# Kernel optimization log

Hardware: AMD Instinct MI355X
Metric: run time of the kernel (lower is better)

## Reference

```python
import jax, jax.numpy as jnp
import numpy as np

B, S, D, H = 2, 2048, 1024, 16
DEPTH = D // H
NEG = -1e9


def setup_inputs() -> dict:
    key = jax.random.key(0)
    ks = jax.random.split(key, 8)
    scale = 1.0 / np.sqrt(D)
    inp = {
        "query": jax.random.normal(ks[0], (B, S, D), jnp.float32),
        "key": jax.random.normal(ks[1], (B, S, D), jnp.float32),
        "value": jax.random.normal(ks[2], (B, S, D), jnp.float32),
        # causal look-ahead mask: 1 where attention is disallowed
        "mask": (1.0 - jnp.tril(jnp.ones((S, S), jnp.float32)))[None, None, :, :],
        "Wq": jax.random.normal(ks[3], (D, D), jnp.float32) * scale,
        "Wk": jax.random.normal(ks[4], (D, D), jnp.float32) * scale,
        "Wv": jax.random.normal(ks[5], (D, D), jnp.float32) * scale,
        "Wo": jax.random.normal(ks[6], (D, D), jnp.float32) * scale,
        "bq": jnp.zeros((D,), jnp.float32),
        "bk": jnp.zeros((D,), jnp.float32),
        "bv": jnp.zeros((D,), jnp.float32),
        "bo": jnp.zeros((D,), jnp.float32),
    }
    return inp


def _split_heads(x):
    # [B,S,D] -> [B,H,S,depth]
    return x.reshape(B, -1, H, DEPTH).transpose(0, 2, 1, 3)


def reference(query, key, value, mask, Wq, Wk, Wv, Wo, bq, bk, bv, bo):
    q = _split_heads(query @ Wq + bq)
    k = _split_heads(key @ Wk + bk)
    v = _split_heads(value @ Wv + bv)
    logits = jnp.einsum("bhqd,bhkd->bhqk", q, k) / jnp.sqrt(jnp.float32(DEPTH))
    logits = logits + mask * NEG
    attn = jax.nn.softmax(logits, axis=-1)
    ctx = jnp.einsum("bhqk,bhkd->bhqd", attn, v)  # [B,H,S,depth]
    concat = ctx.transpose(0, 2, 1, 3).reshape(B, -1, D)
    return concat @ Wo + bo
```

## Files before the change

### kernel.cpp

```cpp
#include <hip/hip_runtime.h>
#include <hip/hip_bf16.h>
#include <stdint.h>

#define BB 2
#define SS 2048
#define DDIM 1024
#define HH 16
#define DEPTH 64
#define MROWS (BB*SS)

typedef short bf16x8 __attribute__((ext_vector_type(8)));
typedef float f32x4 __attribute__((ext_vector_type(4)));

__device__ inline ushort f2bf(float f) {
  union { float f; unsigned u; } v; v.f = f;
  unsigned r = v.u + 0x7fffu + ((v.u >> 16) & 1u);
  return (ushort)(r >> 16);
}

__device__ inline uint pkbf(float a, float b) {
  uint r;
  asm("v_cvt_pk_bf16_f32 %0, %1, %2" : "=v"(r) : "v"(a), "v"(b));
  return r;
}

__device__ inline void gload_lds16(const void* g, void* l) {
  __builtin_amdgcn_global_load_lds(
      (const __attribute__((address_space(1))) unsigned*)g,
      (__attribute__((address_space(3))) unsigned*)l,
      16, 0, 0);
}

__global__ void wprep_kernel(const float* __restrict__ W0, const float* __restrict__ W1,
                             const float* __restrict__ W2, const float* __restrict__ W3,
                             ushort* __restrict__ T0, ushort* __restrict__ T1,
                             ushort* __restrict__ T2, ushort* __restrict__ T3) {
  __shared__ float tile[32][33];
  int z = blockIdx.x >> 10;
  int rr = blockIdx.x & 1023;
  const float* W = (z == 0) ? W0 : (z == 1) ? W1 : (z == 2) ? W2 : W3;
  ushort* T = (z == 0) ? T0 : (z == 1) ? T1 : (z == 2) ? T2 : T3;
  int tx = threadIdx.x & 31, ty = threadIdx.x >> 5;
  int n0 = (rr & 31) * 32, k0 = (rr >> 5) * 32;
#pragma unroll
  for (int i = 0; i < 4; i++)
    tile[ty + i * 8][tx] = W[(size_t)(k0 + ty + i * 8) * DDIM + n0 + tx];
  __syncthreads();
#pragma unroll
  for (int i = 0; i < 4; i++)
    T[(size_t)(n0 + ty + i * 8) * DDIM + k0 + tx] = f2bf(tile[tx][ty + i * 8]);
}

__global__ __launch_bounds__(256, 3) void qkv_gemm_kernel(
    const float* __restrict__ Aq, const float* __restrict__ Ak, const float* __restrict__ Av,
    const ushort* __restrict__ Wqt, const ushort* __restrict__ Wkt, const ushort* __restrict__ Wvt,
    const float* __restrict__ bqp, const float* __restrict__ bkp, const float* __restrict__ bvp,
    ushort* __restrict__ Qh, ushort* __restrict__ Kh, ushort* __restrict__ Vtg) {
  const int id = blockIdx.x;
  const int xcd = id & 7;
  const int rest = id >> 3;
  const int xblk = rest & 7;
  const int slot = rest >> 3;
  const int g = xcd * 12 + slot;
  const int yblk = g & 31;
  const int z = g >> 5;

  const float*  Ap = (z == 0) ? Aq  : (z == 1) ? Ak  : Av;
  const ushort* Bt = (z == 0) ? Wqt : (z == 1) ? Wkt : Wvt;
  const float* bias = (z == 0) ? bqp : (z == 1) ? bkp : bvp;

  __shared__ __align__(16) ushort As[128 * 64];
  __shared__ __align__(16) ushort Bs[2][128 * 64];
  const int tid = threadIdx.x;
  const int w = tid >> 6, lane = tid & 63;
  const int m0 = yblk * 128, n0 = xblk * 128;
  const int wr = (w >> 1) * 64, wc = (w & 1) * 64;
  const int l4 = lane >> 4, l15 = lane & 15;
  const int row16 = tid >> 4;
  const int col4 = (tid & 15) * 4;
  const int srow8 = w * 8 + (lane >> 3);
  const int scol8 = (lane & 7) * 8;

  f32x4 zero = {0.f, 0.f, 0.f, 0.f};
  f32x4 acc[4][4];
#pragma unroll
  for (int i = 0; i < 4; i++)
#pragma unroll
    for (int j = 0; j < 4; j++) acc[i][j] = zero;

  float4 areg[8];
#pragma unroll
  for (int j = 0; j < 8; ++j)
    areg[j] = *(const float4*)&Ap[(size_t)(m0 + j * 16 + row16) * DDIM + col4];
#pragma unroll
  for (int it = 0; it < 4; ++it)
    gload_lds16(Bt + (size_t)(n0 + it * 32 + srow8) * DDIM + scol8,
                &Bs[0][(it * 32 + w * 8) * 64]);
#pragma unroll
  for (int j = 0; j < 8; ++j) {
    uint2 pk;
    pk.x = pkbf(areg[j].x, areg[j].y);
    pk.y = pkbf(areg[j].z, areg[j].w);
    *(uint2*)&As[(j * 16 + row16) * 64 + col4] = pk;
  }
  __syncthreads();

  int buf = 0;
  for (int t = 0; t < 16; ++t) {
    if (t + 1 < 16) {
#pragma unroll
      for (int it = 0; it < 4; ++it)
        gload_lds16(Bt + (size_t)(n0 + it * 32 + srow8) * DDIM + (t + 1) * 64 + scol8,
                    &Bs[buf ^ 1][(it * 32 + w * 8) * 64]);
#pragma unroll
      for (int j = 0; j < 8; ++j)
        areg[j] = *(const float4*)&Ap[(size_t)(m0 + j * 16 + row16) * DDIM + (t + 1) * 64 + col4];
    }
#pragma unroll
    for (int kk = 0; kk < 2; ++kk) {
      bf16x8 af[4], bfr[4];
#pragma unroll
      for (int m = 0; m < 4; m++)
        af[m] = *(const bf16x8*)&As[(wr + m * 16 + l15) * 64 + kk * 32 + l4 * 8];
#pragma unroll
      for (int n = 0; n < 4; n++)
        bfr[n] = *(const bf16x8*)&Bs[buf][(wc + n * 16 + l15) * 64 + kk * 32 + l4 * 8];
#pragma unroll
      for (int m = 0; m < 4; m++)
#pragma unroll
        for (int n = 0; n < 4; n++)
          acc[m][n] = __builtin_amdgcn_mfma_f32_16x16x32_bf16(af[m], bfr[n], acc[m][n], 0, 0, 0);
    }
    __syncthreads();
    if (t + 1 < 16) {
#pragma unroll
      for (int j = 0; j < 8; ++j) {
        uint2 pk;
        pk.x = pkbf(areg[j].x, areg[j].y);
        pk.y = pkbf(areg[j].z, areg[j].w);
        *(uint2*)&As[(j * 16 + row16) * 64 + col4] = pk;
      }
    }
    __syncthreads();
    buf ^= 1;
  }

  if (z != 2) {
    ushort* outp = (z == 0) ? Qh : Kh;
    ushort* wtile = (w < 2) ? &As[w * 4096] : &Bs[0][(w - 2) * 4096];
    const int gcol0 = n0 + wc;
    const int hh = gcol0 >> 6;
    const int bb = m0 >> 11;
    const int s0g = (m0 + wr) & (SS - 1);
#pragma unroll
    for (int m = 0; m < 4; m++) {
#pragma unroll
      for (int n = 0; n < 4; n++) {
        int dloc = n * 16 + l15;
        float bv = bias[gcol0 + dloc];
#pragma unroll
        for (int r = 0; r < 4; r++) {
          int sloc = m * 16 + l4 * 4 + r;
          wtile[sloc * 64 + (dloc ^ ((sloc & 7) << 3))] = f2bf(acc[m][n][r] + bv);
        }
      }
    }
#pragma unroll
    for (int i = 0; i < 8; ++i) {
      int srow = i * 8 + (lane >> 3);
      int dch = (lane & 7) * 8;
      bf16x8 val = *(const bf16x8*)&wtile[srow * 64 + (dch ^ ((srow & 7) << 3))];
      *(bf16x8*)&outp[((size_t)(bb * HH + hh) * SS + s0g + srow) * DEPTH + dch] = val;
    }
  } else {
    ushort* wtile = (w < 2) ? &As[w * 2048] : &Bs[0][(w - 2) * 2048];
    const int gcol0 = n0 + wc;
    const int hh = gcol0 >> 6;
    const int bb = m0 >> 11;
    const int s0g = (m0 + wr) & (SS - 1);
#pragma unroll
    for (int p = 0; p < 2; ++p) {
#pragma unroll
      for (int nn = 0; nn < 2; ++nn) {
        int n = p * 2 + nn;
        int dloc = nn * 16 + l15;
        float bv = bias[gcol0 + p * 32 + dloc];
#pragma unroll
        for (int m = 0; m < 4; m++) {
#pragma unroll
          for (int rr = 0; rr < 4; rr += 2) {
            int sloc = m * 16 + l4 * 4 + rr;
            int gg = (sloc >> 3) ^ (dloc & 7);
            uint pk = pkbf(acc[m][n][rr] + bv, acc[m][n][rr + 1] + bv);
            *(uint*)&wtile[dloc * 64 + gg * 8 + (sloc & 7)] = pk;
          }
        }
      }
      __syncthreads();
#pragma unroll
      for (int i = 0; i < 4; ++i) {
        int dloc = (lane >> 3) + i * 8;
        int gg = (lane & 7) ^ (dloc & 7);
        bf16x8 val = *(const bf16x8*)&wtile[dloc * 64 + gg * 8];
        int dglob = p * 32 + dloc;
        size_t addr = ((size_t)(bb * HH + hh) * DEPTH + dglob) * SS + s0g + (lane & 7) * 8;
        *(bf16x8*)&Vtg[addr] = val;
      }
      __syncthreads();
    }
  }
}

__global__ __launch_bounds__(256, 3) void out_gemm_kernel(
    const ushort* __restrict__ A, const ushort* __restrict__ Bt,
    const float* __restrict__ bias, float* __restrict__ out,
    int M, int N, int K) {
  __shared__ __align__(16) ushort As[2][128 * 64];
  __shared__ __align__(16) ushort Bs[2][64 * 64];
  const int id = blockIdx.x;
  const int xcd = id & 7;
  const int rest = id >> 3;
  const int xblk = rest & 15;
  const int slot = rest >> 4;
  const int yblk = xcd * 4 + slot;

  const int tid = threadIdx.x;
  const int w = tid >> 6, lane = tid & 63;
  const int m0 = yblk * 128, n0 = xblk * 64;
  const int wr = (w >> 1) * 64, wc = (w & 1) * 32;
  const int l4 = lane >> 4, l15 = lane & 15;
  const int srow8 = w * 8 + (lane >> 3);
  const int scol8 = (lane & 7) * 8;

  f32x4 zero = {0.f, 0.f, 0.f, 0.f};
  f32x4 acc[4][2];
#pragma unroll
  for (int i = 0; i < 4; i++)
#pragma unroll
    for (int j = 0; j < 2; j++) acc[i][j] = zero;

#pragma unroll
  for (int it = 0; it < 4; ++it)
    gload_lds16(A + (size_t)(m0 + it * 32 + srow8) * K + scol8,
                &As[0][(it * 32 + w * 8) * 64]);
#pragma unroll
  for (int it = 0; it < 2; ++it)
    gload_lds16(Bt + (size_t)(n0 + it * 32 + srow8) * K + scol8,
                &Bs[0][(it * 32 + w * 8) * 64]);
  __syncthreads();

  int buf = 0;
  for (int t = 0; t < 16; ++t) {
    if (t + 1 < 16) {
#pragma unroll
      for (int it = 0; it < 4; ++it)
        gload_lds16(A + (size_t)(m0 + it * 32 + srow8) * K + (t + 1) * 64 + scol8,
                    &As[buf ^ 1][(it * 32 + w * 8) * 64]);
#pragma unroll
      for (int it = 0; it < 2; ++it)
        gload_lds16(Bt + (size_t)(n0 + it * 32 + srow8) * K + (t + 1) * 64 + scol8,
                    &Bs[buf ^ 1][(it * 32 + w * 8) * 64]);
    }
#pragma unroll
    for (int kk = 0; kk < 2; ++kk) {
      bf16x8 af[4], bfr[2];
#pragma unroll
      for (int m = 0; m < 4; m++)
        af[m] = *(const bf16x8*)&As[buf][(wr + m * 16 + l15) * 64 + kk * 32 + l4 * 8];
#pragma unroll
      for (int n = 0; n < 2; n++)
        bfr[n] = *(const bf16x8*)&Bs[buf][(wc + n * 16 + l15) * 64 + kk * 32 + l4 * 8];
#pragma unroll
      for (int m = 0; m < 4; m++)
#pragma unroll
        for (int n = 0; n < 2; n++)
          acc[m][n] = __builtin_amdgcn_mfma_f32_16x16x32_bf16(af[m], bfr[n], acc[m][n], 0, 0, 0);
    }
    __syncthreads();
    buf ^= 1;
  }

#pragma unroll
  for (int m = 0; m < 4; m++) {
#pragma unroll
    for (int n = 0; n < 2; n++) {
      int col = n0 + wc + n * 16 + l15;
      float bv = bias[col];
#pragma unroll
      for (int r = 0; r < 4; r++) {
        int row = m0 + wr + m * 16 + l4 * 4 + r;
        out[(size_t)row * N + col] = acc[m][n][r] + bv;
      }
    }
  }
}

__global__ __launch_bounds__(256, 4) void attn_kernel(
    const ushort* __restrict__ Qh, const ushort* __restrict__ Kh,
    const ushort* __restrict__ Vt, ushort* __restrict__ ctx) {
  __shared__ __align__(16) ushort Ks[2][64 * 64];
  __shared__ __align__(16) ushort Vs[2][64 * 64];
  __shared__ __align__(16) ushort Ps[4][16 * 64];
  const int tid = threadIdx.x;
  const int w = tid >> 6, lane = tid & 63;
  const int l4 = lane >> 4, l15 = lane & 15;
  const float CE = 0.18033688f;

  const int xcd = blockIdx.x & 7;
  const int local = blockIdx.x >> 3;
  const int bh = xcd * 4 + (local & 3);
  const int chunk = 31 - (local >> 2);
  const int b = bh >> 4, h = bh & 15;
  const size_t qkbase = (size_t)bh * SS * DEPTH;
  const size_t vbase  = (size_t)bh * DEPTH * SS;

  const int srow_w = w * 8 + (lane >> 3);
  const int colb_lin = (lane & 7) * 16;
  const int swz_rd = (l15 & 7) << 3;

  const int q0 = chunk * 64 + w * 16;
  const int nt = chunk + 1;

  const int krow0 = srow_w;
  const int kcol  = (colb_lin ^ ((krow0 & 7) << 4)) >> 1;
  const ushort* kp0 = Kh + qkbase + (size_t)krow0 * DEPTH + kcol;
  const ushort* kp1 = kp0 + 32 * DEPTH;
  const ushort* vp0 = Vt + vbase + (size_t)krow0 * SS + kcol;
  const ushort* vp1 = vp0 + 32 * SS;
  const int lds0 = w * 512;
  const int lds1 = 2048 + w * 512;

  bf16x8 aq[2];
#pragma unroll
  for (int cc = 0; cc < 2; cc++)
    aq[cc] = *(const bf16x8*)&Qh[qkbase + (size_t)(q0 + l15) * DEPTH + cc * 32 + l4 * 8];

  f32x4 zero = {0.f, 0.f, 0.f, 0.f};
  f32x4 o[4];
  float m_run = -__builtin_inff(), l_run = 0.f;
#pragma unroll
  for (int d = 0; d < 4; d++) o[d] = zero;

  int buf = 0;
  gload_lds16(kp0, &Ks[0][lds0]);
  gload_lds16(vp0, &Vs[0][lds0]);
  gload_lds16(kp1, &Ks[0][lds1]);
  gload_lds16(vp1, &Vs[0][lds1]);
  kp0 += 64 * DEPTH; kp1 += 64 * DEPTH; vp0 += 64; vp1 += 64;
  __syncthreads();

  for (int t = 0; t < nt; ++t) {
    if (t + 1 < nt) {
      gload_lds16(kp0, &Ks[buf ^ 1][lds0]);
      gload_lds16(vp0, &Vs[buf ^ 1][lds0]);
      gload_lds16(kp1, &Ks[buf ^ 1][lds1]);
      gload_lds16(vp1, &Vs[buf ^ 1][lds1]);
      kp0 += 64 * DEPTH; kp1 += 64 * DEPTH; vp0 += 64; vp1 += 64;
    }

    const int kv0 = t * 64;
    f32x4 s[4];
    __builtin_amdgcn_s_setprio(1);
#pragma unroll
    for (int n = 0; n < 4; n++) {
      f32x4 zacc = zero;
      int kr = n * 16 + l15;
#pragma unroll
      for (int cc = 0; cc < 2; cc++) {
        bf16x8 bk = *(const bf16x8*)&Ks[buf][kr * 64 + ((cc * 32 + l4 * 8) ^ swz_rd)];
        zacc = __builtin_amdgcn_mfma_f32_16x16x32_bf16(bk, aq[cc], zacc, 0, 0, 0);
      }
      s[n] = zacc;
    }
    __builtin_amdgcn_s_setprio(0);

    const int qg = q0 + l15;
    if (t == nt - 1) {
#pragma unroll
      for (int n = 0; n < 4; n++) {
        int kb = kv0 + n * 16 + l4 * 4;
#pragma unroll
        for (int r = 0; r < 4; r++)
          if (kb + r > qg) s[n][r] = -1e9f;
      }
    }

    float mx = fmaxf(fmaxf(s[0][0], s[0][1]), s[0][2]);
    mx = fmaxf(fmaxf(mx, s[0][3]), s[1][0]);
    mx = fmaxf(fmaxf(mx, s[1][1]), s[1][2]);
    mx = fmaxf(fmaxf(mx, s[1][3]), s[2][0]);
    mx = fmaxf(fmaxf(mx, s[2][1]), s[2][2]);
    mx = fmaxf(fmaxf(mx, s[2][3]), s[3][0]);
    mx = fmaxf(fmaxf(mx, s[3][1]), s[3][2]);
    mx = fmaxf(mx, s[3][3]);
    mx = fmaxf(mx, __shfl_xor(mx, 16));
    mx = fmaxf(mx, __shfl_xor(mx, 32));
    if (!__all(mx - m_run <= 44.36f)) {
      float mnew = fmaxf(m_run, mx);
      float alpha = exp2f((m_run - mnew) * CE);
      m_run = mnew;
      l_run *= alpha;
#pragma unroll
      for (int d = 0; d < 4; d++) o[d] *= alpha;
    }
    float mc = m_run * CE;
    float rs = 0.f;
#pragma unroll
    for (int n = 0; n < 4; n++)
#pragma unroll
      for (int r = 0; r < 4; r++) {
        float p = exp2f(s[n][r] * CE - mc);
        s[n][r] = p;
        rs += p;
      }
    l_run += rs;

    ushort* Pw = &Ps[w][0];
#pragma unroll
    for (int n = 0; n < 4; n++) {
      int col = (n * 16 + l4 * 4) ^ swz_rd;
      uint2 pk;
      pk.x = pkbf(s[n][0], s[n][1]);
      pk.y = pkbf(s[n][2], s[n][3]);
      *(uint2*)&Pw[l15 * 64 + col] = pk;
    }

    bf16x8 pa[2];
#pragma unroll
    for (int cc = 0; cc < 2; cc++)
      pa[cc] = *(const bf16x8*)&Pw[l15 * 64 + ((cc * 32 + l4 * 8) ^ swz_rd)];

    __builtin_amdgcn_s_setprio(1);
#pragma unroll
    for (int d = 0; d < 4; d++) {
      int dr = d * 16 + l15;
#pragma unroll
      for (int cc = 0; cc < 2; cc++) {
        bf16x8 av = *(const bf16x8*)&Vs[buf][dr * 64 + ((cc * 32 + l4 * 8) ^ swz_rd)];
        o[d] = __builtin_amdgcn_mfma_f32_16x16x32_bf16(av, pa[cc], o[d], 0, 0, 0);
      }
    }
    __builtin_amdgcn_s_setprio(0);

    __syncthreads();
    buf ^= 1;
  }

  float lv = l_run;
  lv += __shfl_xor(lv, 16);
  lv += __shfl_xor(lv, 32);
  float inv = 1.f / lv;
  size_t rowbase = ((size_t)(b * SS + q0 + l15)) * DDIM + h * DEPTH;
#pragma unroll
  for (int d = 0; d < 4; d++) {
    *(uint*)&ctx[rowbase + d * 16 + l4 * 4]     = pkbf(o[d][0] * inv, o[d][1] * inv);
    *(uint*)&ctx[rowbase + d * 16 + l4 * 4 + 2] = pkbf(o[d][2] * inv, o[d][3] * inv);
  }
}

extern "C" void kernel_launch(void* const* d_in, const int* in_sizes, int n_in,
                              void* d_out, int out_size, void* d_ws, size_t ws_size,
                              hipStream_t stream) {
  const float* query = (const float*)d_in[0];
  const float* key_  = (const float*)d_in[1];
  const float* value = (const float*)d_in[2];
  const float* Wq = (const float*)d_in[4];
  const float* Wk = (const float*)d_in[5];
  const float* Wv = (const float*)d_in[6];
  const float* Wo = (const float*)d_in[7];
  const float* bq = (const float*)d_in[8];
  const float* bk = (const float*)d_in[9];
  const float* bv = (const float*)d_in[10];
  const float* bo = (const float*)d_in[11];

  char* ws = (char*)d_ws;
  const size_t MB = 1u << 20;
  ushort* Wqt = (ushort*)(ws + 24 * MB);
  ushort* Wkt = (ushort*)(ws + 26 * MB);
  ushort* Wvt = (ushort*)(ws + 28 * MB);
  ushort* Wot = (ushort*)(ws + 30 * MB);
  ushort* Qh  = (ushort*)(ws + 32 * MB);
  ushort* Kh  = (ushort*)(ws + 40 * MB);
  ushort* Vtg = (ushort*)(ws + 48 * MB);
  ushort* Cb  = (ushort*)(ws + 56 * MB);

  wprep_kernel<<<4096, 256, 0, stream>>>(Wq, Wk, Wv, Wo, Wqt, Wkt, Wvt, Wot);

  qkv_gemm_kernel<<<768, 256, 0, stream>>>(
      query, key_, value, Wqt, Wkt, Wvt, bq, bk, bv, Qh, Kh, Vtg);

  attn_kernel<<<1024, 256, 0, stream>>>(Qh, Kh, Vtg, Cb);

  out_gemm_kernel<<<512, 256, 0, stream>>>(
      Cb, Wot, bo, (float*)d_out, MROWS, DDIM, DDIM);
}
```

Baseline: 115.8 us.

## Deepen A-operand prefetch to two stages with manual waitcnt scheduling in projection GEMM

Restructures the QKV projection GEMM main loop so fp32 A-tile global loads are issued two K-steps ahead, alternating between two register sets, while B tiles keep a one-step LDS double buffer. Explicit s_waitcnt counts, raw s_barrier and sched_barrier pin the order of loads, MFMAs and LDS writes in place of __syncthreads, and the loop is unrolled by two with a hand-written tail. The aim is to hide global load latency behind MFMA work. In exchange it doubles the A prefetch registers, which may lower occupancy, and the hard-coded vmcnt values make correctness depend on exact instruction counts.

Measured after the change: 154.6 us. +33.5%, slower.

```diff
diff --git a/kernel.cpp b/kernel.cpp
--- a/kernel.cpp
+++ b/kernel.cpp
@@ -30,6 +30,8 @@
       (__attribute__((address_space(3))) unsigned*)l,
       16, 0, 0);
 }
+
+#define SBAR()  __builtin_amdgcn_sched_barrier(0)
 
 __global__ void wprep_kernel(const float* __restrict__ W0, const float* __restrict__ W1,
                              const float* __restrict__ W2, const float* __restrict__ W3,
@@ -88,62 +90,95 @@
 #pragma unroll
     for (int j = 0; j < 4; j++) acc[i][j] = zero;
 
-  float4 areg[8];
-#pragma unroll
-  for (int j = 0; j < 8; ++j)
-    areg[j] = *(const float4*)&Ap[(size_t)(m0 + j * 16 + row16) * DDIM + col4];
-#pragma unroll
-  for (int it = 0; it < 4; ++it)
-    gload_lds16(Bt + (size_t)(n0 + it * 32 + srow8) * DDIM + scol8,
-                &Bs[0][(it * 32 + w * 8) * 64]);
-#pragma unroll
-  for (int j = 0; j < 8; ++j) {
-    uint2 pk;
-    pk.x = pkbf(areg[j].x, areg[j].y);
-    pk.y = pkbf(areg[j].z, areg[j].w);
-    *(uint2*)&As[(j * 16 + row16) * 64 + col4] = pk;
+  float4 aregA[8], aregB[8];
+
+#define ISSUE_A(T, AR) do {                                                     \
+  _Pragma("unroll")                                                             \
+  for (int j = 0; j < 8; ++j)                                                   \
+    AR[j] = *(const float4*)&Ap[(size_t)(m0 + j * 16 + row16) * DDIM + (T) * 64 + col4]; \
+  SBAR();                                                                       \
+} while (0)
+
+#define ISSUE_B(T, S) do {                                                      \
+  _Pragma("unroll")                                                             \
+  for (int it = 0; it < 4; ++it)                                                \
+    gload_lds16(Bt + (size_t)(n0 + it * 32 + srow8) * DDIM + (T) * 64 + scol8,  \
+                &Bs[S][(it * 32 + w * 8) * 64]);                                \
+  SBAR();                                                                       \
+} while (0)
+
+#define WRITE_A(AR) do {                                                        \
+  _Pragma("unroll")                                                             \
+  for (int j = 0; j < 8; ++j) {                                                 \
+    uint2 pk;                                                                   \
+    pk.x = pkbf(AR[j].x, AR[j].y);                                              \
+    pk.y = pkbf(AR[j].z, AR[j].w);                                              \
+    *(uint2*)&As[(j * 16 + row16) * 64 + col4] = pk;                            \
+  }                                                                             \
+} while (0)
+
+#define MFMA_T(S) do {                                                          \
+  _Pragma("unroll")                                                             \
+  for (int kk = 0; kk < 2; ++kk) {                                              \
+    bf16x8 af[4], bfr[4];                                                       \
+    _Pragma("unroll")                                                           \
+    for (int m = 0; m < 4; m++)                                                 \
+      af[m] = *(const bf16x8*)&As[(wr + m * 16 + l15) * 64 + kk * 32 + l4 * 8]; \
+    _Pragma("unroll")                                                           \
+    for (int n = 0; n < 4; n++)                                                 \
+      bfr[n] = *(const bf16x8*)&Bs[S][(wc + n * 16 + l15) * 64 + kk * 32 + l4 * 8]; \
+    _Pragma("unroll")                                                           \
+    for (int m = 0; m < 4; m++)                                                 \
+      _Pragma("unroll")                                                         \
+      for (int n = 0; n < 4; n++)                                               \
+        acc[m][n] = __builtin_amdgcn_mfma_f32_16x16x32_bf16(af[m], bfr[n], acc[m][n], 0, 0, 0); \
+  }                                                                             \
+} while (0)
+
+#define STEP(T, ARcur, ARnext) do {                                             \
+  ISSUE_B((T) + 1, buf ^ 1);                                                    \
+  ISSUE_A((T) + 2, ARnext);                                                     \
+  MFMA_T(buf);                                                                  \
+  asm volatile("s_waitcnt vmcnt(12)"); SBAR();                                  \
+  asm volatile("s_waitcnt lgkmcnt(0)"); SBAR();                                 \
+  __builtin_amdgcn_s_barrier(); SBAR();                                         \
+  WRITE_A(ARcur);                                                               \
+  asm volatile("s_waitcnt vmcnt(8) lgkmcnt(0)"); SBAR();                        \
+  __builtin_amdgcn_s_barrier(); SBAR();                                         \
+  buf ^= 1;                                                                     \
+} while (0)
+
+  ISSUE_A(0, aregA);
+  ISSUE_B(0, 0);
+  asm volatile("s_waitcnt vmcnt(4)"); SBAR();
+  WRITE_A(aregA);
+  ISSUE_A(1, aregA);
+  asm volatile("s_waitcnt vmcnt(8) lgkmcnt(0)"); SBAR();
+  __builtin_amdgcn_s_barrier(); SBAR();
+
+  int buf = 0;
+  for (int tt = 0; tt < 14; tt += 2) {
+    STEP(tt,     aregA, aregB);
+    STEP(tt + 1, aregB, aregA);
   }
-  __syncthreads();
-
-  int buf = 0;
-  for (int t = 0; t < 16; ++t) {
-    if (t + 1 < 16) {
-#pragma unroll
-      for (int it = 0; it < 4; ++it)
-        gload_lds16(Bt + (size_t)(n0 + it * 32 + srow8) * DDIM + (t + 1) * 64 + scol8,
-                    &Bs[buf ^ 1][(it * 32 + w * 8) * 64]);
-#pragma unroll
-      for (int j = 0; j < 8; ++j)
-        areg[j] = *(const float4*)&Ap[(size_t)(m0 + j * 16 + row16) * DDIM + (t + 1) * 64 + col4];
-    }
-#pragma unroll
-    for (int kk = 0; kk < 2; ++kk) {
-      bf16x8 af[4], bfr[4];
-#pragma unroll
-      for (int m = 0; m < 4; m++)
-        af[m] = *(const bf16x8*)&As[(wr + m * 16 + l15) * 64 + kk * 32 + l4 * 8];
-#pragma unroll
-      for (int n = 0; n < 4; n++)
-        bfr[n] = *(const bf16x8*)&Bs[buf][(wc + n * 16 + l15) * 64 + kk * 32 + l4 * 8];
-#pragma unroll
-      for (int m = 0; m < 4; m++)
-#pragma unroll
-        for (int n = 0; n < 4; n++)
-          acc[m][n] = __builtin_amdgcn_mfma_f32_16x16x32_bf16(af[m], bfr[n], acc[m][n], 0, 0, 0);
-    }
-    __syncthreads();
-    if (t + 1 < 16) {
-#pragma unroll
-      for (int j = 0; j < 8; ++j) {
-        uint2 pk;
-        pk.x = pkbf(areg[j].x, areg[j].y);
-        pk.y = pkbf(areg[j].z, areg[j].w);
-        *(uint2*)&As[(j * 16 + row16) * 64 + col4] = pk;
-      }
-    }
-    __syncthreads();
-    buf ^= 1;
-  }
+  ISSUE_B(15, buf ^ 1);
+  MFMA_T(buf);
+  asm volatile("s_waitcnt vmcnt(4)"); SBAR();
+  asm volatile("s_waitcnt lgkmcnt(0)"); SBAR();
+  __builtin_amdgcn_s_barrier(); SBAR();
+  WRITE_A(aregA);
+  asm volatile("s_waitcnt vmcnt(0) lgkmcnt(0)"); SBAR();
+  __builtin_amdgcn_s_barrier(); SBAR();
+  buf ^= 1;
+  MFMA_T(buf);
+  asm volatile("s_waitcnt lgkmcnt(0)"); SBAR();
+  __builtin_amdgcn_s_barrier(); SBAR();
+
+#undef STEP
+#undef MFMA_T
+#undef WRITE_A
+#undef ISSUE_B
+#undef ISSUE_A
 
   if (z != 2) {
     ushort* outp = (z == 0) ? Qh : Kh;
```
